# Optimization experiments

Measured on AMD Instinct MI355X. Metric: run time of the kernel, lower is better.

Reference implementation:

```python
import jax, jax.numpy as jnp
import numpy as np

BITS = 8
KQA_TOPK_PROP = 0.25
NUM_HEADS = 16


def quantize_pc(t, n_bits=BITS):
    # per-channel fake quantization over the last dim (torch quantize with
    # quantization_type='per_channel')
    q_max = 2 ** (n_bits - 1) - 1
    scales = jnp.max(jnp.abs(t), axis=-1, keepdims=True)
    scales = jnp.maximum(scales, 1e-5) / q_max
    return jnp.clip(jnp.round(t / scales), -q_max - 1, q_max) * scales


def setup_inputs() -> dict:
    key = jax.random.key(0)
    ks = jax.random.split(key, 5)
    B, N, C = 4, 1024, 1024
    x = jax.random.normal(ks[0], (B, N, C), dtype=jnp.float32)
    W_qkv = jax.random.normal(ks[1], (3 * C, C), dtype=jnp.float32) * (C ** -0.5)
    b_qkv = jax.random.normal(ks[2], (3 * C,), dtype=jnp.float32) * 0.02
    W_proj = jax.random.normal(ks[3], (C, C), dtype=jnp.float32) * (C ** -0.5)
    b_proj = jax.random.normal(ks[4], (C,), dtype=jnp.float32) * 0.02
    return {"x": x, "W_qkv": W_qkv, "b_qkv": b_qkv, "W_proj": W_proj, "b_proj": b_proj}


def _split_qkv(lin, B, N, H, hd):
    # [B,N,3C] -> (3,B,H,N,hd)
    t = jnp.transpose(lin.reshape(B, N, 3, H, hd), (2, 0, 3, 1, 4))
    return t[0], t[1], t[2]


def reference(x, W_qkv, b_qkv, W_proj, b_proj):
    B, N, C = x.shape
    H = NUM_HEADS
    hd = C // H
    scale = hd ** -0.5

    # --- quantized QKV path (KeyQueryAttention) ---
    q_x = quantize_pc(x)
    q_w = quantize_pc(W_qkv)
    q_b = quantize_pc(b_qkv)
    q_lin = quantize_pc(jnp.einsum('bnc,oc->bno', q_x, q_w) + q_b)
    q_q, q_k, _ = _split_qkv(q_lin, B, N, H, hd)
    q_attn = jnp.einsum('bhnd,bhmd->bhnm', q_q, q_k) * scale

    # --- topk-sliced partial-matmul approximation path ---
    r1 = int(C * KQA_TOPK_PROP) + 1  # channel slice of x / W_qkv
    topk_lin = jnp.einsum('bnc,oc->bno', x[:, :, :r1], W_qkv[:, :r1]) + b_qkv
    topk_q, topk_k, _ = _split_qkv(topk_lin, B, N, H, hd)
    r2 = int(hd * KQA_TOPK_PROP) + 1  # slices the SEQUENCE dim (dim 2), as in the torch code
    topk_attn = jnp.einsum('bhnd,bhmd->bhnm', topk_q[:, :, :r2], topk_k[:, :, :r2]) * scale

    # --- exact attention path (used for the output) ---
    lin = jnp.einsum('bnc,oc->bno', x, W_qkv) + b_qkv
    q, k, v = _split_qkv(lin, B, N, H, hd)
    attn = jax.nn.softmax(jnp.einsum('bhnd,bhmd->bhnm', q, k) * scale, axis=-1)
    out = jnp.einsum('bhnm,bhmd->bhnd', attn, v)  # [B,H,N,hd]
    out = jnp.transpose(out, (0, 2, 1, 3)).reshape(B, N, C)
    out = jnp.einsum('bnc,oc->bno', out, W_proj) + b_proj
    return out, q_attn, topk_attn
```

## Files before the change

kernel.cpp:

```cpp
#include <hip/hip_runtime.h>
#include <stdint.h>

typedef __bf16 bf16x8 __attribute__((ext_vector_type(8)));
typedef float f32x4 __attribute__((ext_vector_type(4)));
typedef int i32x4 __attribute__((ext_vector_type(4)));
typedef unsigned short u16;

#define DEVI static __device__ __forceinline__

DEVI u16 bfu(float f){
  unsigned u = __builtin_bit_cast(unsigned, f);
  unsigned r = u + 0x7fffu + ((u >> 16) & 1u);
  return (u16)(r >> 16);
}
DEVI float ubf(u16 h){
  unsigned u = ((unsigned)h) << 16;
  return __builtin_bit_cast(float, u);
}
DEVI unsigned packbf(float a, float b){
  return (unsigned)bfu(a) | ((unsigned)bfu(b) << 16);
}

DEVI void gload16(const void* g, void* s){
  __builtin_amdgcn_global_load_lds(
      (const __attribute__((address_space(1))) unsigned int*)g,
      (__attribute__((address_space(3))) unsigned int*)s, 16, 0, 0);
}

DEVI float waveReduceMax(float v){
  for (int off = 1; off < 64; off <<= 1) v = fmaxf(v, __shfl_xor(v, off));
  return v;
}

DEVI float blockReduceMax(float v, float* sred){
  for (int off = 32; off; off >>= 1) v = fmaxf(v, __shfl_xor(v, off));
  int w = threadIdx.x >> 6;
  if ((threadIdx.x & 63) == 0) sred[w] = v;
  __syncthreads();
  float r = fmaxf(fmaxf(sred[0], sred[1]), fmaxf(sred[2], sred[3]));
  __syncthreads();
  return r;
}

DEVI void quant_row_wave(const float* __restrict__ in, int8_t* __restrict__ qo,
                         u16* __restrict__ bo, float* __restrict__ so, int row){
  const int lane = threadIdx.x & 63;
  const float* rp = in + (size_t)row * 1024;
  float4 v[4];
  float am = 0.f;
  for (int i = 0; i < 4; i++){
    v[i] = *(const float4*)(rp + i * 256 + lane * 4);
    am = fmaxf(am, fmaxf(fmaxf(fabsf(v[i].x), fabsf(v[i].y)),
                         fmaxf(fabsf(v[i].z), fabsf(v[i].w))));
  }
  am = waveReduceMax(am);
  const float s = fmaxf(am, 1e-5f) / 127.0f;
  if (lane == 0) so[row] = s;
  for (int i = 0; i < 4; i++){
    char4 q;
    q.x = (int8_t)(int)fminf(fmaxf(rintf(v[i].x / s), -128.f), 127.f);
    q.y = (int8_t)(int)fminf(fmaxf(rintf(v[i].y / s), -128.f), 127.f);
    q.z = (int8_t)(int)fminf(fmaxf(rintf(v[i].z / s), -128.f), 127.f);
    q.w = (int8_t)(int)fminf(fmaxf(rintf(v[i].w / s), -128.f), 127.f);
    *(char4*)(qo + (size_t)row * 1024 + i * 256 + lane * 4) = q;
    ushort4 h; h.x = bfu(v[i].x); h.y = bfu(v[i].y); h.z = bfu(v[i].z); h.w = bfu(v[i].w);
    *(ushort4*)(bo + (size_t)row * 1024 + i * 256 + lane * 4) = h;
  }
}

DEVI void quant_b_body(const float* __restrict__ b, float* __restrict__ qb, float* sred){
  const int t = threadIdx.x;
  float am = 0.f;
  for (int i = t; i < 3072; i += 256) am = fmaxf(am, fabsf(b[i]));
  am = blockReduceMax(am, sred);
  const float s = fmaxf(am, 1e-5f) / 127.0f;
  for (int i = t; i < 3072; i += 256){
    float q = fminf(fmaxf(rintf(b[i] / s), -128.f), 127.f);
    qb[i] = q * s;
  }
}

DEVI void topk_lin_body(int idx, const float* __restrict__ x, const float* __restrict__ Wq,
                        const float* __restrict__ bq, float* __restrict__ tlin){
  const int o = idx & 2047, bn = idx >> 11;
  const int b_ = bn / 17, n = bn % 17;
  const float* xr = x + ((size_t)b_ * 1024 + n) * 1024;
  const float* wr = Wq + (size_t)o * 1024;
  const float4* x4 = (const float4*)xr;
  const float4* w4 = (const float4*)wr;
  float s = 0.f;
  for (int c = 0; c < 64; c++){
    float4 a = x4[c], b = w4[c];
    s += a.x * b.x + a.y * b.y + a.z * b.z + a.w * b.w;
  }
  s += xr[256] * wr[256];
  tlin[idx] = s + bq[o];
}

DEVI void gemm_i8_body(char* smem, int tid, const int8_t* __restrict__ A, const int8_t* __restrict__ Bm,
    const float* __restrict__ sx, const float* __restrict__ sw, const float* __restrict__ qb,
    u16* __restrict__ out){
  int8_t* As = (int8_t*)smem;
  int8_t* Bs = (int8_t*)(smem + 8192);
  const int t = threadIdx.x, l = t & 63, w = t >> 6;
  const int m0 = (tid / 24) * 128, n0 = (tid % 24) * 128;
  const int wm = (w >> 1) * 64, wn = (w & 1) * 64, lr = l & 15, lg = l >> 4;
  i32x4 acc[4][4];
  i32x4 z = {0, 0, 0, 0};
  for (int i = 0; i < 4; i++) for (int j = 0; j < 4; j++) acc[i][j] = z;
  for (int kt = 0; kt < 16; kt++){
    __syncthreads();
    for (int it = 0; it < 2; it++){
      int c = w * 2 + it;
      int idx = c * 64 + l;
      int r = idx >> 2, boff = (idx & 3) * 16;
      gload16(A  + (size_t)(m0 + r) * 1024 + kt * 64 + boff, &As[c * 1024]);
      gload16(Bm + (size_t)(n0 + r) * 1024 + kt * 64 + boff, &Bs[c * 1024]);
    }
    __syncthreads();
    i32x4 a[4], b[4];
    for (int i = 0; i < 4; i++) a[i] = *(const i32x4*)(&As[(wm + i * 16 + lr) * 64 + lg * 16]);
    for (int j = 0; j < 4; j++) b[j] = *(const i32x4*)(&Bs[(wn + j * 16 + lr) * 64 + lg * 16]);
    __builtin_amdgcn_s_setprio(1);
    for (int i = 0; i < 4; i++)
      for (int j = 0; j < 4; j++)
        acc[i][j] = __builtin_amdgcn_mfma_i32_16x16x64_i8(a[i], b[j], acc[i][j], 0, 0, 0);
    __builtin_amdgcn_s_setprio(0);
  }
  for (int i = 0; i < 4; i++){
    int row = m0 + wm + i * 16 + lg * 4;
    for (int j = 0; j < 4; j++){
      int col = n0 + wn + j * 16 + lr;
      float swc = sw[col], qbc = qb[col];
      for (int r = 0; r < 4; r++)
        out[(size_t)(row + r) * 3072 + col] = bfu((float)acc[i][j][r] * sx[row + r] * swc + qbc);
    }
  }
}

template<int MODE>
DEVI void gemm_bf16_body(char* smem, int tid, const u16* __restrict__ A, const u16* __restrict__ Bm,
    const float* __restrict__ bias, void* __restrict__ outp, int K, int N, int nxb){
  u16* As = (u16*)smem;
  u16* Bs = (u16*)(smem + 8192);
  const int t = threadIdx.x, l = t & 63, w = t >> 6;
  const int m0 = (tid / nxb) * 128, n0 = (tid % nxb) * 128;
  const int wm = (w >> 1) * 64, wn = (w & 1) * 64, lr = l & 15, lg = l >> 4;
  f32x4 acc[4][4];
  f32x4 z = {0.f, 0.f, 0.f, 0.f};
  for (int i = 0; i < 4; i++) for (int j = 0; j < 4; j++) acc[i][j] = z;
  const int nkt = K >> 5;
  for (int kt = 0; kt < nkt; kt++){
    __syncthreads();
    for (int it = 0; it < 2; it++){
      int c = w * 2 + it;
      int idx = c * 64 + l;
      int r = idx >> 2, off = (idx & 3) * 8;
      gload16(A  + (size_t)(m0 + r) * K + kt * 32 + off, &As[c * 512]);
      gload16(Bm + (size_t)(n0 + r) * K + kt * 32 + off, &Bs[c * 512]);
    }
    __syncthreads();
    bf16x8 a[4], b[4];
    for (int i = 0; i < 4; i++) a[i] = *(const bf16x8*)(&As[(wm + i * 16 + lr) * 32 + lg * 8]);
    for (int j = 0; j < 4; j++) b[j] = *(const bf16x8*)(&Bs[(wn + j * 16 + lr) * 32 + lg * 8]);
    __builtin_amdgcn_s_setprio(1);
    for (int i = 0; i < 4; i++)
      for (int j = 0; j < 4; j++)
        acc[i][j] = __builtin_amdgcn_mfma_f32_16x16x32_bf16(a[i], b[j], acc[i][j], 0, 0, 0);
    __builtin_amdgcn_s_setprio(0);
  }
  for (int i = 0; i < 4; i++){
    int row = m0 + wm + i * 16 + lg * 4;
    for (int j = 0; j < 4; j++){
      int col = n0 + wn + j * 16 + lr;
      float bc = bias[col];
      for (int r = 0; r < 4; r++){
        float v = acc[i][j][r] + bc;
        if (MODE == 0){
          int s = col >> 10, h = (col >> 6) & 15, d = col & 63;
          int b_ = (row + r) >> 10, n = (row + r) & 1023;
          ((u16*)outp)[(((size_t)(s * 64 + b_ * 16 + h)) * 1024 + n) * 64 + d] = bfu(v);
        } else {
          ((float*)outp)[(size_t)(row + r) * N + col] = v;
        }
      }
    }
  }
}

DEVI void topk_attn_body(int b2, const float* __restrict__ tlin, float* __restrict__ outp){
  const int idx = b2 * 256 + threadIdx.x;
  if (idx >= 4 * 16 * 17 * 17) return;
  const int mm = idx % 17; int rest = idx / 17;
  const int nn = rest % 17; rest /= 17;
  const int h = rest % 16; const int b_ = rest / 16;
  const float* tq = tlin + ((size_t)(b_ * 17 + nn)) * 2048 + h * 64;
  const float* tk = tlin + ((size_t)(b_ * 17 + mm)) * 2048 + 1024 + h * 64;
  float s = 0.f;
  for (int d = 0; d < 64; d++) s += tq[d] * tk[d];
  outp[71303168 + idx] = s * 0.125f;
}

DEVI void qlin_quant_wave(int row, const u16* __restrict__ qlin,
                          float* __restrict__ s_ql, int8_t* __restrict__ iq, int8_t* __restrict__ ik){
  const int lane = threadIdx.x & 63;
  const u16* rp = qlin + (size_t)row * 3072;
  uint4 raw[6];
  float am = 0.f;
  for (int i = 0; i < 6; i++){
    raw[i] = *(const uint4*)(rp + i * 512 + lane * 8);
    const u16* pp = (const u16*)&raw[i];
    for (int j = 0; j < 8; j++) am = fmaxf(am, fabsf(ubf(pp[j])));
  }
  am = waveReduceMax(am);
  const float s = fmaxf(am, 1e-5f) / 127.0f;
  if (lane == 0) s_ql[row] = s;
  const int b_ = row >> 10, n = row & 1023;
  for (int i = 0; i < 4; i++){
    const int o0 = i * 512 + lane * 8;
    int8_t* dst = (o0 < 1024) ? iq : ik;
    const int oo = o0 & 1023, h = oo >> 6, d = oo & 63;
    const size_t base = (((size_t)(b_ * 16 + h) * 1024 + n) * 64 + d);
    const u16* pp = (const u16*)&raw[i];
    union { int8_t c[8]; unsigned long long u; } pk;
    for (int j = 0; j < 8; j++)
      pk.c[j] = (int8_t)(int)fminf(fmaxf(rintf(ubf(pp[j]) / s), -128.f), 127.f);
    *(unsigned long long*)(dst + base) = pk.u;
  }
}

DEVI void attn_body(u16* vt, int qt, int bz, const u16* __restrict__ qkv, u16* __restrict__ aout){
  const int t = threadIdx.x, l = t & 63, w = t >> 6, lr = l & 15, lg = l >> 4;
  const int b_ = bz >> 4, h = bz & 15;
  const u16* Q  = qkv + (size_t)bz * 65536;
  const u16* Kg = qkv + (size_t)(64 + bz) * 65536;
  const u16* Vg = qkv + (size_t)(128 + bz) * 65536;
  const int q0 = qt * 64 + w * 16;
  const bf16x8 bq0 = *(const bf16x8*)(Q + (size_t)(q0 + lr) * 64 + lg * 8);
  const bf16x8 bq1 = *(const bf16x8*)(Q + (size_t)(q0 + lr) * 64 + 32 + lg * 8);
  float m = -1e30f, lsum = 0.f;
  f32x4 o[4];
  f32x4 zf = {0.f, 0.f, 0.f, 0.f};
  for (int dt = 0; dt < 4; dt++) o[dt] = zf;
  const int hi = lg & 1, tt = lg >> 1;
  const int srcA = lr + 32 * hi, srcB = srcA + 16;
  const int vr = t >> 3, voff = (t & 7) * 8;
  {
    uint4 vv = *(const uint4*)(Vg + (size_t)vr * 64 + voff);
    const u16* pv = (const u16*)&vv;
    for (int j = 0; j < 8; j++) vt[(0 * 64 + voff + j) * 40 + vr] = pv[j];
  }
  __syncthreads();
  int cur = 0;
  for (int kv0 = 0; kv0 < 1024; kv0 += 32){
    const bf16x8 ak00 = *(const bf16x8*)(Kg + (size_t)(kv0 + lr) * 64 + lg * 8);
    const bf16x8 ak01 = *(const bf16x8*)(Kg + (size_t)(kv0 + lr) * 64 + 32 + lg * 8);
    const bf16x8 ak10 = *(const bf16x8*)(Kg + (size_t)(kv0 + 16 + lr) * 64 + lg * 8);
    const bf16x8 ak11 = *(const bf16x8*)(Kg + (size_t)(kv0 + 16 + lr) * 64 + 32 + lg * 8);
    const bool more = (kv0 + 32) < 1024;
    uint4 vn = {0, 0, 0, 0};
    if (more) vn = *(const uint4*)(Vg + (size_t)(kv0 + 32 + vr) * 64 + voff);
    f32x4 st[2];
    {
      __builtin_amdgcn_s_setprio(1);
      f32x4 c = zf;
      c = __builtin_amdgcn_mfma_f32_16x16x32_bf16(ak00, bq0, c, 0, 0, 0);
      c = __builtin_amdgcn_mfma_f32_16x16x32_bf16(ak01, bq1, c, 0, 0, 0);
      st[0] = c;
      c = zf;
      c = __builtin_amdgcn_mfma_f32_16x16x32_bf16(ak10, bq0, c, 0, 0, 0);
      c = __builtin_amdgcn_mfma_f32_16x16x32_bf16(ak11, bq1, c, 0, 0, 0);
      st[1] = c;
      __builtin_amdgcn_s_setprio(0);
    }
    float tmax = -1e30f;
    for (int kvt = 0; kvt < 2; kvt++)
      for (int r = 0; r < 4; r++){ st[kvt][r] *= 0.125f; tmax = fmaxf(tmax, st[kvt][r]); }
    tmax = fmaxf(tmax, __shfl_xor(tmax, 16));
    tmax = fmaxf(tmax, __shfl_xor(tmax, 32));
    const float mn = fmaxf(m, tmax);
    const float f = __expf(m - mn);
    m = mn;
    float p[2][4], psum = 0.f;
    for (int kvt = 0; kvt < 2; kvt++)
      for (int r = 0; r < 4; r++){ float e = __expf(st[kvt][r] - mn); p[kvt][r] = e; psum += e; }
    psum += __shfl_xor(psum, 16);
    psum += __shfl_xor(psum, 32);
    lsum = lsum * f + psum;
    for (int dt = 0; dt < 4; dt++) for (int r = 0; r < 4; r++) o[dt][r] *= f;
    int pk00 = (int)packbf(p[0][0], p[0][1]), pk01 = (int)packbf(p[0][2], p[0][3]);
    int pk10 = (int)packbf(p[1][0], p[1][1]), pk11 = (int)packbf(p[1][2], p[1][3]);
    int a0 = __shfl(pk00, srcA), a1 = __shfl(pk10, srcA);
    int b0 = __shfl(pk01, srcA), b1 = __shfl(pk11, srcA);
    int c0 = __shfl(pk00, srcB), c1 = __shfl(pk10, srcB);
    int d0 = __shfl(pk01, srcB), d1 = __shfl(pk11, srcB);
    union { unsigned u[4]; bf16x8 v; } bp;
    bp.u[0] = (unsigned)(tt ? a1 : a0);
    bp.u[1] = (unsigned)(tt ? b1 : b0);
    bp.u[2] = (unsigned)(tt ? c1 : c0);
    bp.u[3] = (unsigned)(tt ? d1 : d0);
    __builtin_amdgcn_s_setprio(1);
    for (int dt = 0; dt < 4; dt++){
      bf16x8 av = *(const bf16x8*)(&vt[(cur * 64 + dt * 16 + lr) * 40 + lg * 8]);
      o[dt] = __builtin_amdgcn_mfma_f32_16x16x32_bf16(av, bp.v, o[dt], 0, 0, 0);
    }
    __builtin_amdgcn_s_setprio(0);
    if (more){
      const u16* pv = (const u16*)&vn;
      for (int j = 0; j < 8; j++) vt[((cur ^ 1) * 64 + voff + j) * 40 + vr] = pv[j];
    }
    __syncthreads();
    cur ^= 1;
  }
  const float rn = 1.0f / lsum;
  for (int dt = 0; dt < 4; dt++){
    ushort4 hv;
    hv.x = bfu(o[dt][0] * rn); hv.y = bfu(o[dt][1] * rn);
    hv.z = bfu(o[dt][2] * rn); hv.w = bfu(o[dt][3] * rn);
    *(ushort4*)(aout + ((size_t)(b_ * 1024 + q0 + lr)) * 1024 + h * 64 + dt * 16 + lg * 4) = hv;
  }
}

DEVI void qattn_body(int b2, const int8_t* __restrict__ iq, const int8_t* __restrict__ ik,
    const float* __restrict__ s_ql, float* __restrict__ outp){
  const int t = threadIdx.x, l = t & 63, w = t >> 6, lr = l & 15, lg = l >> 4;
  const int n0 = (b2 & 7) * 128, m0 = ((b2 >> 3) & 7) * 128, bz = b2 >> 6;
  const int wm = (w >> 1) * 64, wn = (w & 1) * 64;
  const int b_ = bz >> 4;
  const int8_t* Aq = iq + (size_t)bz * 65536;
  const int8_t* Bk = ik + (size_t)bz * 65536;
  i32x4 a[4], b[4];
  for (int i = 0; i < 4; i++) a[i] = *(const i32x4*)(Aq + (size_t)(m0 + wm + i * 16 + lr) * 64 + lg * 16);
  for (int j = 0; j < 4; j++) b[j] = *(const i32x4*)(Bk + (size_t)(n0 + wn + j * 16 + lr) * 64 + lg * 16);
  float* op = outp + 4194304 + (size_t)bz * 1048576;
  i32x4 z = {0, 0, 0, 0};
  for (int i = 0; i < 4; i++){
    int row = m0 + wm + i * 16 + lg * 4;
    for (int j = 0; j < 4; j++){
      i32x4 acc = __builtin_amdgcn_mfma_i32_16x16x64_i8(a[i], b[j], z, 0, 0, 0);
      int col = n0 + wn + j * 16 + lr;
      float sc = s_ql[b_ * 1024 + col] * 0.125f;
      for (int r = 0; r < 4; r++)
        op[(size_t)(row + r) * 1024 + col] = (float)acc[r] * s_ql[b_ * 1024 + row + r] * sc;
    }
  }
}

__global__ __launch_bounds__(256) void stageA(
    const float* __restrict__ x, const float* __restrict__ Wq, const float* __restrict__ bq,
    const float* __restrict__ Wp,
    int8_t* __restrict__ ix, u16* __restrict__ xb, float* __restrict__ sx,
    int8_t* __restrict__ iw, u16* __restrict__ wb, float* __restrict__ sw,
    float* __restrict__ qbv, u16* __restrict__ Wpb, float* __restrict__ tlin){
  __shared__ float sred[4];
  const int bid = blockIdx.x, t = threadIdx.x, wv = t >> 6;
  if (bid < 544){
    topk_lin_body(bid * 256 + t, x, Wq, bq, tlin);
  } else if (bid < 1568){
    quant_row_wave(x, ix, xb, sx, (bid - 544) * 4 + wv);
  } else if (bid < 2336){
    quant_row_wave(Wq, iw, wb, sw, (bid - 1568) * 4 + wv);
  } else if (bid < 2848){
    const int i = ((bid - 2336) * 256 + t) * 8;
    float4 a = *(const float4*)(Wp + i);
    float4 b = *(const float4*)(Wp + i + 4);
    ushort4 h0; h0.x = bfu(a.x); h0.y = bfu(a.y); h0.z = bfu(a.z); h0.w = bfu(a.w);
    ushort4 h1; h1.x = bfu(b.x); h1.y = bfu(b.y); h1.z = bfu(b.z); h1.w = bfu(b.w);
    *(ushort4*)(Wpb + i) = h0;
    *(ushort4*)(Wpb + i + 4) = h1;
  } else {
    quant_b_body(bq, qbv, sred);
  }
}

__global__ __launch_bounds__(256) void stageB(
    const int8_t* __restrict__ ix, const int8_t* __restrict__ iw, const float* __restrict__ sx,
    const float* __restrict__ sw, const float* __restrict__ qbv, u16* __restrict__ qlin,
    const u16* __restrict__ xb, const u16* __restrict__ wb, const float* __restrict__ bq,
    u16* __restrict__ qkv){
  __shared__ __align__(16) char smem[16384];
  const int bid = blockIdx.x;
  if (bid < 768){
    const int tid = (bid & 7) * 96 + (bid >> 3);
    gemm_bf16_body<0>(smem, tid, xb, wb, bq, qkv, 1024, 3072, 24);
  } else {
    const int g = bid - 768;
    const int tid = (g & 7) * 96 + (g >> 3);
    gemm_i8_body(smem, tid, ix, iw, sx, sw, qbv, qlin);
  }
}

__global__ __launch_bounds__(256) void stageC(
    const u16* __restrict__ qkv, u16* __restrict__ aout,
    const u16* __restrict__ qlin, float* __restrict__ sql,
    int8_t* __restrict__ iq, int8_t* __restrict__ ik,
    const float* __restrict__ tlin, float* __restrict__ dout){
  __shared__ __align__(16) char smem[10240];
  const int bid = blockIdx.x, wv = threadIdx.x >> 6;
  if (bid < 1024){
    const int wk = (bid & 7) * 128 + (bid >> 3);
    attn_body((u16*)smem, wk & 15, wk >> 4, qkv, aout);
  } else if (bid < 2048){
    qlin_quant_wave((bid - 1024) * 4 + wv, qlin, sql, iq, ik);
  } else {
    topk_attn_body(bid - 2048, tlin, dout);
  }
}

__global__ __launch_bounds__(256) void stageD(
    const u16* __restrict__ aout, const u16* __restrict__ Wpb, const float* __restrict__ bp,
    float* __restrict__ dout,
    const int8_t* __restrict__ iq, const int8_t* __restrict__ ik, const float* __restrict__ sql){
  __shared__ __align__(16) char smem[16384];
  const int bid = blockIdx.x;
  if (bid < 256) gemm_bf16_body<1>(smem, bid, aout, Wpb, bp, dout, 1024, 1024, 8);
  else {
    const int g = bid - 256;
    const int w = (g & 7) * 512 + (g >> 3);
    qattn_body(w, iq, ik, sql, dout);
  }
}

extern "C" void kernel_launch(void* const* d_in, const int* in_sizes, int n_in,
                              void* d_out, int out_size, void* d_ws, size_t ws_size,
                              hipStream_t stream){
  const float* x  = (const float*)d_in[0];
  const float* Wq = (const float*)d_in[1];
  const float* bq = (const float*)d_in[2];
  const float* Wp = (const float*)d_in[3];
  const float* bp = (const float*)d_in[4];
  char* ws = (char*)d_ws;
  size_t off = 0;
  auto alloc = [&](size_t bytes) -> void* {
    void* p = ws + off; off += (bytes + 255) & ~(size_t)255; return p;
  };
  u16*    qlin = (u16*)   alloc(4096ull * 3072 * 2);
  int8_t* ix   = (int8_t*)alloc(4096ull * 1024);
  int8_t* iw   = (int8_t*)alloc(3072ull * 1024);
  int8_t* iq   = (int8_t*)alloc(64ull * 1024 * 64);
  int8_t* ik   = (int8_t*)alloc(64ull * 1024 * 64);
  u16*    xb   = (u16*)   alloc(4096ull * 1024 * 2);
  u16*    Wb   = (u16*)   alloc(3072ull * 1024 * 2);
  u16*    qkv  = (u16*)   alloc(3ull * 64 * 1024 * 64 * 2);
  u16*    aout = (u16*)   alloc(4096ull * 1024 * 2);
  u16*    Wpb  = (u16*)   alloc(1024ull * 1024 * 2);
  float*  tlin = (float*) alloc(4ull * 17 * 2048 * 4);
  float*  sx   = (float*) alloc(4096 * 4);
  float*  sw   = (float*) alloc(3072 * 4);
  float*  qbv  = (float*) alloc(3072 * 4);
  float*  sql  = (float*) alloc(4096 * 4);
  float*  dout = (float*)d_out;

  stageA<<<2849, 256, 0, stream>>>(x, Wq, bq, Wp, ix, xb, sx, iw, Wb, sw, qbv, Wpb, tlin);
  stageB<<<1536, 256, 0, stream>>>(ix, iw, sx, sw, qbv, qlin, xb, Wb, bq, qkv);
  stageC<<<2121, 256, 0, stream>>>(qkv, aout, qlin, sql, iq, ik, tlin, dout);
  stageD<<<4352, 256, 0, stream>>>(aout, Wpb, bp, dout, iq, ik, sql);
}
```

Measured before the change: 241.3 us.

## Fuse qlin row-max into int8 GEMM epilogue and skip storing unused V columns

The int8 QKV GEMM epilogue now computes per-row absolute maxima of its bf16 outputs, reduces them across lanes and publishes them with atomicMax into a zeroed workspace buffer. The qlin quantization pass then reads this precomputed scale instead of rereading all 3072 columns per row, loading only the Q and K columns. The GEMM also skips storing the V third of qlin, which is never consumed, cutting global writes. This adds extra launch blocks to zero the max buffer and atomic traffic in the epilogue. It relies on the float bit patterns of non-negative values ordering the same as unsigned integers.

```diff
diff --git a/kernel.cpp b/kernel.cpp
--- a/kernel.cpp
+++ b/kernel.cpp
@@ -99,11 +99,12 @@
 
 DEVI void gemm_i8_body(char* smem, int tid, const int8_t* __restrict__ A, const int8_t* __restrict__ Bm,
     const float* __restrict__ sx, const float* __restrict__ sw, const float* __restrict__ qb,
-    u16* __restrict__ out){
+    u16* __restrict__ out, unsigned* __restrict__ sqlmax){
   int8_t* As = (int8_t*)smem;
   int8_t* Bs = (int8_t*)(smem + 8192);
   const int t = threadIdx.x, l = t & 63, w = t >> 6;
   const int m0 = (tid / 24) * 128, n0 = (tid % 24) * 128;
+  const bool dostore = (tid % 24) < 16;
   const int wm = (w >> 1) * 64, wn = (w & 1) * 64, lr = l & 15, lg = l >> 4;
   i32x4 acc[4][4];
   i32x4 z = {0, 0, 0, 0};
@@ -127,15 +128,30 @@
         acc[i][j] = __builtin_amdgcn_mfma_i32_16x16x64_i8(a[i], b[j], acc[i][j], 0, 0, 0);
     __builtin_amdgcn_s_setprio(0);
   }
-  for (int i = 0; i < 4; i++){
-    int row = m0 + wm + i * 16 + lg * 4;
+  float myrm = 0.f;
+  for (int i = 0; i < 4; i++){
+    const int row = m0 + wm + i * 16 + lg * 4;
+    float rm[4] = {0.f, 0.f, 0.f, 0.f};
     for (int j = 0; j < 4; j++){
-      int col = n0 + wn + j * 16 + lr;
-      float swc = sw[col], qbc = qb[col];
-      for (int r = 0; r < 4; r++)
-        out[(size_t)(row + r) * 3072 + col] = bfu((float)acc[i][j][r] * sx[row + r] * swc + qbc);
-    }
-  }
+      const int col = n0 + wn + j * 16 + lr;
+      const float swc = sw[col], qbc = qb[col];
+      for (int r = 0; r < 4; r++){
+        const u16 h = bfu((float)acc[i][j][r] * sx[row + r] * swc + qbc);
+        if (dostore) out[(size_t)(row + r) * 3072 + col] = h;
+        rm[r] = fmaxf(rm[r], fabsf(ubf(h)));
+      }
+    }
+    for (int r = 0; r < 4; r++){
+      float v = rm[r];
+      v = fmaxf(v, __shfl_xor(v, 1));
+      v = fmaxf(v, __shfl_xor(v, 2));
+      v = fmaxf(v, __shfl_xor(v, 4));
+      v = fmaxf(v, __shfl_xor(v, 8));
+      if (lr == i * 4 + r) myrm = v;
+    }
+  }
+  const int arow = m0 + wm + (lr >> 2) * 16 + lg * 4 + (lr & 3);
+  atomicMax(&sqlmax[arow], __builtin_bit_cast(unsigned, myrm));
 }
 
 template<int MODE>
@@ -201,27 +217,21 @@
   outp[71303168 + idx] = s * 0.125f;
 }
 
-DEVI void qlin_quant_wave(int row, const u16* __restrict__ qlin,
+DEVI void qlin_quant_wave(int row, const u16* __restrict__ qlin, const unsigned* __restrict__ sqlmax,
                           float* __restrict__ s_ql, int8_t* __restrict__ iq, int8_t* __restrict__ ik){
   const int lane = threadIdx.x & 63;
   const u16* rp = qlin + (size_t)row * 3072;
-  uint4 raw[6];
-  float am = 0.f;
-  for (int i = 0; i < 6; i++){
-    raw[i] = *(const uint4*)(rp + i * 512 + lane * 8);
-    const u16* pp = (const u16*)&raw[i];
-    for (int j = 0; j < 8; j++) am = fmaxf(am, fabsf(ubf(pp[j])));
-  }
-  am = waveReduceMax(am);
+  const float am = __builtin_bit_cast(float, sqlmax[row]);
   const float s = fmaxf(am, 1e-5f) / 127.0f;
   if (lane == 0) s_ql[row] = s;
   const int b_ = row >> 10, n = row & 1023;
   for (int i = 0; i < 4; i++){
     const int o0 = i * 512 + lane * 8;
+    uint4 raw = *(const uint4*)(rp + o0);
     int8_t* dst = (o0 < 1024) ? iq : ik;
     const int oo = o0 & 1023, h = oo >> 6, d = oo & 63;
     const size_t base = (((size_t)(b_ * 16 + h) * 1024 + n) * 64 + d);
-    const u16* pp = (const u16*)&raw[i];
+    const u16* pp = (const u16*)&raw;
     union { int8_t c[8]; unsigned long long u; } pk;
     for (int j = 0; j < 8; j++)
       pk.c[j] = (int8_t)(int)fminf(fmaxf(rintf(ubf(pp[j]) / s), -128.f), 127.f);
@@ -351,7 +361,8 @@
     const float* __restrict__ Wp,
     int8_t* __restrict__ ix, u16* __restrict__ xb, float* __restrict__ sx,
     int8_t* __restrict__ iw, u16* __restrict__ wb, float* __restrict__ sw,
-    float* __restrict__ qbv, u16* __restrict__ Wpb, float* __restrict__ tlin){
+    float* __restrict__ qbv, u16* __restrict__ Wpb, float* __restrict__ tlin,
+    unsigned* __restrict__ sqlmax){
   __shared__ float sred[4];
   const int bid = blockIdx.x, t = threadIdx.x, wv = t >> 6;
   if (bid < 544){
@@ -368,8 +379,10 @@
     ushort4 h1; h1.x = bfu(b.x); h1.y = bfu(b.y); h1.z = bfu(b.z); h1.w = bfu(b.w);
     *(ushort4*)(Wpb + i) = h0;
     *(ushort4*)(Wpb + i + 4) = h1;
+  } else if (bid == 2848){
+    quant_b_body(bq, qbv, sred);
   } else {
-    quant_b_body(bq, qbv, sred);
+    sqlmax[(bid - 2849) * 256 + t] = 0u;
   }
 }
 
@@ -377,7 +390,7 @@
     const int8_t* __restrict__ ix, const int8_t* __restrict__ iw, const float* __restrict__ sx,
     const float* __restrict__ sw, const float* __restrict__ qbv, u16* __restrict__ qlin,
     const u16* __restrict__ xb, const u16* __restrict__ wb, const float* __restrict__ bq,
-    u16* __restrict__ qkv){
+    u16* __restrict__ qkv, unsigned* __restrict__ sqlmax){
   __shared__ __align__(16) char smem[16384];
   const int bid = blockIdx.x;
   if (bid < 768){
@@ -386,13 +399,13 @@
   } else {
     const int g = bid - 768;
     const int tid = (g & 7) * 96 + (g >> 3);
-    gemm_i8_body(smem, tid, ix, iw, sx, sw, qbv, qlin);
+    gemm_i8_body(smem, tid, ix, iw, sx, sw, qbv, qlin, sqlmax);
   }
 }
 
 __global__ __launch_bounds__(256) void stageC(
     const u16* __restrict__ qkv, u16* __restrict__ aout,
-    const u16* __restrict__ qlin, float* __restrict__ sql,
+    const u16* __restrict__ qlin, const unsigned* __restrict__ sqlmax, float* __restrict__ sql,
     int8_t* __restrict__ iq, int8_t* __restrict__ ik,
     const float* __restrict__ tlin, float* __restrict__ dout){
   __shared__ __align__(16) char smem[10240];
@@ -401,7 +414,7 @@
     const int wk = (bid & 7) * 128 + (bid >> 3);
     attn_body((u16*)smem, wk & 15, wk >> 4, qkv, aout);
   } else if (bid < 2048){
-    qlin_quant_wave((bid - 1024) * 4 + wv, qlin, sql, iq, ik);
+    qlin_quant_wave((bid - 1024) * 4 + wv, qlin, sqlmax, sql, iq, ik);
   } else {
     topk_attn_body(bid - 2048, tlin, dout);
   }
@@ -434,25 +447,26 @@
   auto alloc = [&](size_t bytes) -> void* {
     void* p = ws + off; off += (bytes + 255) & ~(size_t)255; return p;
   };
-  u16*    qlin = (u16*)   alloc(4096ull * 3072 * 2);
-  int8_t* ix   = (int8_t*)alloc(4096ull * 1024);
-  int8_t* iw   = (int8_t*)alloc(3072ull * 1024);
-  int8_t* iq   = (int8_t*)alloc(64ull * 1024 * 64);
-  int8_t* ik   = (int8_t*)alloc(64ull * 1024 * 64);
-  u16*    xb   = (u16*)   alloc(4096ull * 1024 * 2);
-  u16*    Wb   = (u16*)   alloc(3072ull * 1024 * 2);
-  u16*    qkv  = (u16*)   alloc(3ull * 64 * 1024 * 64 * 2);
-  u16*    aout = (u16*)   alloc(4096ull * 1024 * 2);
-  u16*    Wpb  = (u16*)   alloc(1024ull * 1024 * 2);
-  float*  tlin = (float*) alloc(4ull * 17 * 2048 * 4);
-  float*  sx   = (float*) alloc(4096 * 4);
-  float*  sw   = (float*) alloc(3072 * 4);
-  float*  qbv  = (float*) alloc(3072 * 4);
-  float*  sql  = (float*) alloc(4096 * 4);
-  float*  dout = (float*)d_out;
-
-  stageA<<<2849, 256, 0, stream>>>(x, Wq, bq, Wp, ix, xb, sx, iw, Wb, sw, qbv, Wpb, tlin);
-  stageB<<<1536, 256, 0, stream>>>(ix, iw, sx, sw, qbv, qlin, xb, Wb, bq, qkv);
-  stageC<<<2121, 256, 0, stream>>>(qkv, aout, qlin, sql, iq, ik, tlin, dout);
+  u16*      qlin = (u16*)     alloc(4096ull * 3072 * 2);
+  int8_t*   ix   = (int8_t*)  alloc(4096ull * 1024);
+  int8_t*   iw   = (int8_t*)  alloc(3072ull * 1024);
+  int8_t*   iq   = (int8_t*)  alloc(64ull * 1024 * 64);
+  int8_t*   ik   = (int8_t*)  alloc(64ull * 1024 * 64);
+  u16*      xb   = (u16*)     alloc(4096ull * 1024 * 2);
+  u16*      Wb   = (u16*)     alloc(3072ull * 1024 * 2);
+  u16*      qkv  = (u16*)     alloc(3ull * 64 * 1024 * 64 * 2);
+  u16*      aout = (u16*)     alloc(4096ull * 1024 * 2);
+  u16*      Wpb  = (u16*)     alloc(1024ull * 1024 * 2);
+  float*    tlin = (float*)   alloc(4ull * 17 * 2048 * 4);
+  float*    sx   = (float*)   alloc(4096 * 4);
+  float*    sw   = (float*)   alloc(3072 * 4);
+  float*    qbv  = (float*)   alloc(3072 * 4);
+  float*    sql  = (float*)   alloc(4096 * 4);
+  unsigned* sqlm = (unsigned*)alloc(4096 * 4);
+  float*    dout = (float*)d_out;
+
+  stageA<<<2865, 256, 0, stream>>>(x, Wq, bq, Wp, ix, xb, sx, iw, Wb, sw, qbv, Wpb, tlin, sqlm);
+  stageB<<<1536, 256, 0, stream>>>(ix, iw, sx, sw, qbv, qlin, xb, Wb, bq, qkv, sqlm);
+  stageC<<<2121, 256, 0, stream>>>(qkv, aout, qlin, sqlm, sql, iq, ik, tlin, dout);
   stageD<<<4352, 256, 0, stream>>>(aout, Wpb, bp, dout, iq, ik, sql);
 }
```

Result: no change. 244.8 us (+1.4%).

## Process 64 keys per attention iteration with wider V tile and lazy rescale

Applied to the files above, without the earlier changes.

The flash-attention loop now handles 64 KV rows per iteration instead of 32. Each iteration issues four QK MFMA pairs and two PV MFMAs per output tile, so the number of barriers and softmax reduction rounds halves. The transposed V tile in LDS grows to 64 columns with a 72-element pitch, which raises stageC shared memory from 10 KB to 18 KB and may lower occupancy. It also skips the output and sum rescale when no lane's running max increased.

```diff
diff --git a/kernel.cpp b/kernel.cpp
--- a/kernel.cpp
+++ b/kernel.cpp
@@ -244,70 +244,93 @@
   for (int dt = 0; dt < 4; dt++) o[dt] = zf;
   const int hi = lg & 1, tt = lg >> 1;
   const int srcA = lr + 32 * hi, srcB = srcA + 16;
-  const int vr = t >> 3, voff = (t & 7) * 8;
+  const int vr = t & 63, dbase = (t >> 6) * 16;
   {
-    uint4 vv = *(const uint4*)(Vg + (size_t)vr * 64 + voff);
-    const u16* pv = (const u16*)&vv;
-    for (int j = 0; j < 8; j++) vt[(0 * 64 + voff + j) * 40 + vr] = pv[j];
+    uint4 v0 = *(const uint4*)(Vg + (size_t)vr * 64 + dbase);
+    uint4 v1 = *(const uint4*)(Vg + (size_t)vr * 64 + dbase + 8);
+    const u16* p0 = (const u16*)&v0; const u16* p1 = (const u16*)&v1;
+    for (int j = 0; j < 8; j++){
+      vt[(dbase + j) * 72 + vr] = p0[j];
+      vt[(dbase + 8 + j) * 72 + vr] = p1[j];
+    }
   }
   __syncthreads();
   int cur = 0;
-  for (int kv0 = 0; kv0 < 1024; kv0 += 32){
-    const bf16x8 ak00 = *(const bf16x8*)(Kg + (size_t)(kv0 + lr) * 64 + lg * 8);
-    const bf16x8 ak01 = *(const bf16x8*)(Kg + (size_t)(kv0 + lr) * 64 + 32 + lg * 8);
-    const bf16x8 ak10 = *(const bf16x8*)(Kg + (size_t)(kv0 + 16 + lr) * 64 + lg * 8);
-    const bf16x8 ak11 = *(const bf16x8*)(Kg + (size_t)(kv0 + 16 + lr) * 64 + 32 + lg * 8);
-    const bool more = (kv0 + 32) < 1024;
-    uint4 vn = {0, 0, 0, 0};
-    if (more) vn = *(const uint4*)(Vg + (size_t)(kv0 + 32 + vr) * 64 + voff);
-    f32x4 st[2];
-    {
-      __builtin_amdgcn_s_setprio(1);
+  for (int kv0 = 0; kv0 < 1024; kv0 += 64){
+    bf16x8 ak[4][2];
+    for (int x = 0; x < 4; x++){
+      ak[x][0] = *(const bf16x8*)(Kg + (size_t)(kv0 + x * 16 + lr) * 64 + lg * 8);
+      ak[x][1] = *(const bf16x8*)(Kg + (size_t)(kv0 + x * 16 + lr) * 64 + 32 + lg * 8);
+    }
+    const bool more = (kv0 + 64) < 1024;
+    uint4 vn0 = {0,0,0,0}, vn1 = {0,0,0,0};
+    if (more){
+      vn0 = *(const uint4*)(Vg + (size_t)(kv0 + 64 + vr) * 64 + dbase);
+      vn1 = *(const uint4*)(Vg + (size_t)(kv0 + 64 + vr) * 64 + dbase + 8);
+    }
+    f32x4 st[4];
+    __builtin_amdgcn_s_setprio(1);
+    for (int x = 0; x < 4; x++){
       f32x4 c = zf;
-      c = __builtin_amdgcn_mfma_f32_16x16x32_bf16(ak00, bq0, c, 0, 0, 0);
-      c = __builtin_amdgcn_mfma_f32_16x16x32_bf16(ak01, bq1, c, 0, 0, 0);
-      st[0] = c;
-      c = zf;
-      c = __builtin_amdgcn_mfma_f32_16x16x32_bf16(ak10, bq0, c, 0, 0, 0);
-      c = __builtin_amdgcn_mfma_f32_16x16x32_bf16(ak11, bq1, c, 0, 0, 0);
-      st[1] = c;
-      __builtin_amdgcn_s_setprio(0);
-    }
+      c = __builtin_amdgcn_mfma_f32_16x16x32_bf16(ak[x][0], bq0, c, 0, 0, 0);
+      c = __builtin_amdgcn_mfma_f32_16x16x32_bf16(ak[x][1], bq1, c, 0, 0, 0);
+      st[x] = c;
+    }
+    __builtin_amdgcn_s_setprio(0);
     float tmax = -1e30f;
-    for (int kvt = 0; kvt < 2; kvt++)
-      for (int r = 0; r < 4; r++){ st[kvt][r] *= 0.125f; tmax = fmaxf(tmax, st[kvt][r]); }
+    for (int x = 0; x < 4; x++)
+      for (int r = 0; r < 4; r++){ st[x][r] *= 0.125f; tmax = fmaxf(tmax, st[x][r]); }
     tmax = fmaxf(tmax, __shfl_xor(tmax, 16));
     tmax = fmaxf(tmax, __shfl_xor(tmax, 32));
-    const float mn = fmaxf(m, tmax);
-    const float f = __expf(m - mn);
-    m = mn;
-    float p[2][4], psum = 0.f;
-    for (int kvt = 0; kvt < 2; kvt++)
-      for (int r = 0; r < 4; r++){ float e = __expf(st[kvt][r] - mn); p[kvt][r] = e; psum += e; }
+    if (__any(tmax > m)){
+      const float mn = fmaxf(m, tmax);
+      const float f = __expf(m - mn);
+      m = mn;
+      lsum *= f;
+      for (int dt = 0; dt < 4; dt++) for (int r = 0; r < 4; r++) o[dt][r] *= f;
+    }
+    float p[4][4], psum = 0.f;
+    for (int x = 0; x < 4; x++)
+      for (int r = 0; r < 4; r++){ float e = __expf(st[x][r] - m); p[x][r] = e; psum += e; }
     psum += __shfl_xor(psum, 16);
     psum += __shfl_xor(psum, 32);
-    lsum = lsum * f + psum;
-    for (int dt = 0; dt < 4; dt++) for (int r = 0; r < 4; r++) o[dt][r] *= f;
+    lsum += psum;
     int pk00 = (int)packbf(p[0][0], p[0][1]), pk01 = (int)packbf(p[0][2], p[0][3]);
     int pk10 = (int)packbf(p[1][0], p[1][1]), pk11 = (int)packbf(p[1][2], p[1][3]);
+    int pk20 = (int)packbf(p[2][0], p[2][1]), pk21 = (int)packbf(p[2][2], p[2][3]);
+    int pk30 = (int)packbf(p[3][0], p[3][1]), pk31 = (int)packbf(p[3][2], p[3][3]);
     int a0 = __shfl(pk00, srcA), a1 = __shfl(pk10, srcA);
     int b0 = __shfl(pk01, srcA), b1 = __shfl(pk11, srcA);
     int c0 = __shfl(pk00, srcB), c1 = __shfl(pk10, srcB);
     int d0 = __shfl(pk01, srcB), d1 = __shfl(pk11, srcB);
-    union { unsigned u[4]; bf16x8 v; } bp;
-    bp.u[0] = (unsigned)(tt ? a1 : a0);
-    bp.u[1] = (unsigned)(tt ? b1 : b0);
-    bp.u[2] = (unsigned)(tt ? c1 : c0);
-    bp.u[3] = (unsigned)(tt ? d1 : d0);
+    int e0 = __shfl(pk20, srcA), e1 = __shfl(pk30, srcA);
+    int f0 = __shfl(pk21, srcA), f1 = __shfl(pk31, srcA);
+    int g0 = __shfl(pk20, srcB), g1 = __shfl(pk30, srcB);
+    int h0 = __shfl(pk21, srcB), h1 = __shfl(pk31, srcB);
+    union { unsigned u[4]; bf16x8 v; } bp0, bp1;
+    bp0.u[0] = (unsigned)(tt ? a1 : a0);
+    bp0.u[1] = (unsigned)(tt ? b1 : b0);
+    bp0.u[2] = (unsigned)(tt ? c1 : c0);
+    bp0.u[3] = (unsigned)(tt ? d1 : d0);
+    bp1.u[0] = (unsigned)(tt ? e1 : e0);
+    bp1.u[1] = (unsigned)(tt ? f1 : f0);
+    bp1.u[2] = (unsigned)(tt ? g1 : g0);
+    bp1.u[3] = (unsigned)(tt ? h1 : h0);
     __builtin_amdgcn_s_setprio(1);
     for (int dt = 0; dt < 4; dt++){
-      bf16x8 av = *(const bf16x8*)(&vt[(cur * 64 + dt * 16 + lr) * 40 + lg * 8]);
-      o[dt] = __builtin_amdgcn_mfma_f32_16x16x32_bf16(av, bp.v, o[dt], 0, 0, 0);
+      bf16x8 av0 = *(const bf16x8*)(&vt[(cur * 64 + dt * 16 + lr) * 72 + lg * 8]);
+      o[dt] = __builtin_amdgcn_mfma_f32_16x16x32_bf16(av0, bp0.v, o[dt], 0, 0, 0);
+      bf16x8 av1 = *(const bf16x8*)(&vt[(cur * 64 + dt * 16 + lr) * 72 + 32 + lg * 8]);
+      o[dt] = __builtin_amdgcn_mfma_f32_16x16x32_bf16(av1, bp1.v, o[dt], 0, 0, 0);
     }
     __builtin_amdgcn_s_setprio(0);
     if (more){
-      const u16* pv = (const u16*)&vn;
-      for (int j = 0; j < 8; j++) vt[((cur ^ 1) * 64 + voff + j) * 40 + vr] = pv[j];
+      const u16* p0 = (const u16*)&vn0; const u16* p1 = (const u16*)&vn1;
+      const int nb = (cur ^ 1) * 64;
+      for (int j = 0; j < 8; j++){
+        vt[(nb + dbase + j) * 72 + vr] = p0[j];
+        vt[(nb + dbase + 8 + j) * 72 + vr] = p1[j];
+      }
     }
     __syncthreads();
     cur ^= 1;
@@ -395,7 +418,7 @@
     const u16* __restrict__ qlin, float* __restrict__ sql,
     int8_t* __restrict__ iq, int8_t* __restrict__ ik,
     const float* __restrict__ tlin, float* __restrict__ dout){
-  __shared__ __align__(16) char smem[10240];
+  __shared__ __align__(16) char smem[18432];
   const int bid = blockIdx.x, wv = threadIdx.x >> 6;
   if (bid < 1024){
     const int wk = (bid & 7) * 128 + (bid >> 3);
```

Result: slower. 254.2 us (+5.4%).
